# Optimization experiments

Measured on AMD Instinct MI355X. Metric: run time of the kernel, lower is better.

Reference implementation:

```python
import jax, jax.numpy as jnp
import numpy as np

N_NODES = 50000
N_EDGES = 800000
IN_DIM, HID_DIM, OUT_DIM = 128, 128, 64


def _sage_conv(x, src, dst, W_l, W_r, b, num_nodes):
    # mean aggregation of source-node features onto destination nodes
    msg = x[src]  # [E, d] gather
    summed = jax.ops.segment_sum(msg, dst, num_segments=num_nodes)  # [N, d]
    deg = jax.ops.segment_sum(jnp.ones((src.shape[0],), dtype=x.dtype), dst,
                              num_segments=num_nodes)  # [N]
    agg = summed / jnp.maximum(deg, 1.0)[:, None]
    # SAGEConv: lin_l(agg) + lin_r(x); bias only on lin_l (PyG default)
    return agg @ W_l + b + x @ W_r


def setup_inputs() -> dict:
    key = jax.random.key(0)
    k = jax.random.split(key, 8)
    def glorot(kk, shape):
        lim = float(np.sqrt(6.0 / (shape[0] + shape[1])))
        return jax.random.uniform(kk, shape, jnp.float32, -lim, lim)
    return {
        "x": jax.random.normal(k[0], (N_NODES, IN_DIM), jnp.float32),
        "edge_index": jax.random.randint(k[1], (2, N_EDGES), 0, N_NODES, jnp.int64),
        "W1_l": glorot(k[2], (IN_DIM, HID_DIM)),
        "W1_r": glorot(k[3], (IN_DIM, HID_DIM)),
        "b1": jnp.zeros((HID_DIM,), jnp.float32),
        "W2_l": glorot(k[4], (HID_DIM, OUT_DIM)),
        "W2_r": glorot(k[5], (HID_DIM, OUT_DIM)),
        "b2": jnp.zeros((OUT_DIM,), jnp.float32),
    }


def reference(x, edge_index, W1_l, W1_r, b1, W2_l, W2_r, b2):
    src, dst = edge_index[0], edge_index[1]
    n = x.shape[0]
    h = _sage_conv(x, src, dst, W1_l, W1_r, b1, n)
    h = jax.nn.relu(h)
    # dropout is identity in eval mode
    out = _sage_conv(h, src, dst, W2_l, W2_r, b2, n)
    return out
```

## Files before the change

kernel.cpp:

```cpp
#include <hip/hip_runtime.h>
#include <hip/hip_bf16.h>


#define BLK 256

typedef __attribute__((ext_vector_type(8))) short short8;
typedef __attribute__((ext_vector_type(4))) float f32x4;

__device__ inline unsigned short f2bf(float f) {
    unsigned int u = __builtin_bit_cast(unsigned int, f);
    u += 0x7fffu + ((u >> 16) & 1u);
    return (unsigned short)(u >> 16);
}
__device__ inline float bf2f(unsigned short h) {
    return __builtin_bit_cast(float, ((unsigned int)h) << 16);
}


__global__ __launch_bounds__(BLK) void deg_count_kernel(const int* __restrict__ dst,
                                                        int E, int* __restrict__ deg) {
    int e = blockIdx.x * BLK + threadIdx.x;
    if (e < E) atomicAdd(&deg[dst[e]], 1);
}

__global__ __launch_bounds__(BLK) void partial_sum_kernel(const int* __restrict__ deg,
                                                          int n, int* __restrict__ partials) {
    __shared__ int s[BLK];
    int t = threadIdx.x;
    int idx = blockIdx.x * BLK + t;
    s[t] = (idx < n) ? deg[idx] : 0;
    __syncthreads();
    for (int o = BLK / 2; o > 0; o >>= 1) {
        if (t < o) s[t] += s[t + o];
        __syncthreads();
    }
    if (t == 0) partials[blockIdx.x] = s[0];
}

__global__ __launch_bounds__(BLK) void scan_partials_kernel(int* __restrict__ partials, int n) {
    __shared__ int s[BLK];
    int t = threadIdx.x;
    int v = (t < n) ? partials[t] : 0;
    s[t] = v;
    __syncthreads();
    int sum = v;
    for (int o = 1; o < BLK; o <<= 1) {
        int other = (t >= o) ? s[t - o] : 0;
        __syncthreads();
        sum += other;
        s[t] = sum;
        __syncthreads();
    }
    if (t < n) partials[t] = sum - v;
}

__global__ __launch_bounds__(BLK) void chunk_scan_kernel(const int* __restrict__ deg,
                                                         const int* __restrict__ partials,
                                                         int n, int* __restrict__ row_start) {
    __shared__ int s[BLK];
    int t = threadIdx.x;
    int idx = blockIdx.x * BLK + t;
    int v = (idx < n) ? deg[idx] : 0;
    s[t] = v;
    __syncthreads();
    int sum = v;
    for (int o = 1; o < BLK; o <<= 1) {
        int other = (t >= o) ? s[t - o] : 0;
        __syncthreads();
        sum += other;
        s[t] = sum;
        __syncthreads();
    }
    if (idx < n) row_start[idx] = (sum - v) + partials[blockIdx.x];
}

__global__ __launch_bounds__(BLK) void fill_xcd_kernel(const int* __restrict__ src,
                                                       const int* __restrict__ dst, int E,
                                                       const int* __restrict__ row_start,
                                                       int* __restrict__ cursor,
                                                       int* __restrict__ csr_src,
                                                       int range, int CH) {
    const int oct = blockIdx.x & 7;
    const int chunk = blockIdx.x >> 3;
    const int lo = oct * range, hi = lo + range;
    int e0 = chunk * CH;
    int e1 = min(E, e0 + CH);
    for (int e = e0 + threadIdx.x; e < e1; e += BLK) {
        int d = dst[e];
        if (d >= lo && d < hi) {
            int pos = atomicAdd(&cursor[d], 1);
            csr_src[row_start[d] + pos] = src[e];
        }
    }
}


__global__ __launch_bounds__(BLK) void f32_to_bf16_kernel(const float* __restrict__ in,
                                                          unsigned short* __restrict__ out,
                                                          int nquad) {
    int i = blockIdx.x * BLK + threadIdx.x;
    if (i >= nquad) return;
    float4 v = ((const float4*)in)[i];
    ushort4 o;
    o.x = f2bf(v.x); o.y = f2bf(v.y); o.z = f2bf(v.z); o.w = f2bf(v.w);
    ((ushort4*)out)[i] = o;
}

__global__ __launch_bounds__(BLK) void pack_all_w_kernel(const float* __restrict__ W1l,
                                                         const float* __restrict__ W1r,
                                                         const float* __restrict__ W2l,
                                                         const float* __restrict__ W2r,
                                                         unsigned short* __restrict__ P1l,
                                                         unsigned short* __restrict__ P1r,
                                                         unsigned short* __restrict__ P2l,
                                                         unsigned short* __restrict__ P2r) {
    int t = blockIdx.x * BLK + threadIdx.x;
    const float* W;
    unsigned short* P;
    int Ncol, local;
    if (t < 16384)      { W = W1l; P = P1l; Ncol = 128; local = t; }
    else if (t < 32768) { W = W1r; P = P1r; Ncol = 128; local = t - 16384; }
    else if (t < 40960) { W = W2l; P = P2l; Ncol = 64;  local = t - 32768; }
    else if (t < 49152) { W = W2r; P = P2r; Ncol = 64;  local = t - 40960; }
    else return;
    int j = local & 7;
    int lane = (local >> 3) & 63;
    int rest = local >> 9;
    int nt = Ncol >> 4;
    int n16 = rest % nt, kb = rest / nt;
    int k = kb * 32 + (lane >> 4) * 8 + j;
    int c = n16 * 16 + (lane & 15);
    P[local] = f2bf(W[(size_t)k * Ncol + c]);
}


__global__ __launch_bounds__(BLK) void agg_mlp_kernel(const unsigned short* __restrict__ feat,
                                                      const int* __restrict__ row_start,
                                                      const int* __restrict__ deg,
                                                      const int* __restrict__ csr_src,
                                                      unsigned short* __restrict__ out,
                                                      int N, int E) {
    const int wave = threadIdx.x >> 6, lane = threadIdx.x & 63;
    const int node = blockIdx.x * (BLK / 64) + wave;
    if (node >= N) return;
    const int start = __builtin_amdgcn_readfirstlane(row_start[node]);
    int cnt = __builtin_amdgcn_readfirstlane(deg[node]);
    cnt = min(cnt, E);
    const float inv = 1.0f / fmaxf((float)cnt, 1.0f);
    const unsigned int* fp = (const unsigned int*)feat;

    float a0 = 0.f, a1 = 0.f;
    for (int base = 0; base < cnt; base += 64) {
        int m = cnt - base;
        if (m > 64) m = 64;
        int idxv = csr_src[start + base + (lane < m ? lane : m - 1)];
        for (int e = 0; e < m; e += 16) {
            unsigned int v[16];
#pragma unroll
            for (int j = 0; j < 16; j++) {
                int ee = e + j;
                int sl = ee < m ? ee : m - 1;
                int s = __builtin_amdgcn_readlane(idxv, sl);
                v[j] = fp[(size_t)s * 64 + lane];
            }
#pragma unroll
            for (int j = 0; j < 16; j++) {
                float w = (e + j < m) ? inv : 0.0f;
                a0 = fmaf(bf2f((unsigned short)v[j]), w, a0);
                a1 = fmaf(bf2f((unsigned short)(v[j] >> 16)), w, a1);
            }
        }
    }
    ((unsigned int*)out)[(size_t)node * 64 + lane] =
        (unsigned int)f2bf(a0) | ((unsigned int)f2bf(a1) << 16);
}


template <int NCOL, bool RELU, bool OUT_BF16>
__global__ __launch_bounds__(BLK) void gemm_dual_kernel(const unsigned short* __restrict__ A1,
                                                        const unsigned short* __restrict__ A2,
                                                        const unsigned short* __restrict__ Pl,
                                                        const unsigned short* __restrict__ Pr,
                                                        const float* __restrict__ bias,
                                                        void* __restrict__ outp, int M) {
    constexpr int NT = NCOL / 16;
    const int wave = threadIdx.x >> 6, lane = threadIdx.x & 63;
    const int r0 = blockIdx.x * 128 + wave * 32;
    const int arow = lane & 15, kgrp = lane >> 4;

    f32x4 acc[2][NT];
#pragma unroll
    for (int h = 0; h < 2; h++)
#pragma unroll
        for (int n = 0; n < NT; n++) acc[h][n] = (f32x4){0.f, 0.f, 0.f, 0.f};

    const int ra = min(r0 + arow, M - 1);
    const int rb = min(r0 + 16 + arow, M - 1);

#pragma unroll
    for (int mat = 0; mat < 2; ++mat) {
        const unsigned short* A = mat ? A2 : A1;
        const unsigned short* P = mat ? Pr : Pl;
        const unsigned short* Aa = A + (size_t)ra * 128 + kgrp * 8;
        const unsigned short* Ab = A + (size_t)rb * 128 + kgrp * 8;
#pragma unroll
        for (int kb = 0; kb < 4; ++kb) {
            short8 afa = *(const short8*)(Aa + kb * 32);
            short8 afb = *(const short8*)(Ab + kb * 32);
            const unsigned short* Pk = P + (size_t)kb * NT * 512 + lane * 8;
#pragma unroll
            for (int n = 0; n < NT; ++n) {
                short8 wf = *(const short8*)(Pk + n * 512);
                acc[0][n] = __builtin_amdgcn_mfma_f32_16x16x32_bf16(afa, wf, acc[0][n], 0, 0, 0);
                acc[1][n] = __builtin_amdgcn_mfma_f32_16x16x32_bf16(afb, wf, acc[1][n], 0, 0, 0);
            }
        }
    }

#pragma unroll
    for (int n = 0; n < NT; ++n) {
        int col = n * 16 + arow;
        float bv = bias[col];
#pragma unroll
        for (int h = 0; h < 2; ++h) {
#pragma unroll
            for (int i = 0; i < 4; ++i) {
                int row = r0 + h * 16 + kgrp * 4 + i;
                if (row < M) {
                    float v = acc[h][n][i] + bv;
                    if (RELU) v = fmaxf(v, 0.f);
                    if (OUT_BF16)
                        ((unsigned short*)outp)[(size_t)row * NCOL + col] = f2bf(v);
                    else
                        ((float*)outp)[(size_t)row * NCOL + col] = v;
                }
            }
        }
    }
}


extern "C" void kernel_launch(void* const* d_in, const int* in_sizes, int n_in,
                              void* d_out, int out_size, void* d_ws, size_t ws_size,
                              hipStream_t stream) {
    const float* x   = (const float*)d_in[0];
    const int*   ei  = (const int*)d_in[1];
    const float* W1l = (const float*)d_in[2];
    const float* W1r = (const float*)d_in[3];
    const float* b1  = (const float*)d_in[4];
    const float* W2l = (const float*)d_in[5];
    const float* W2r = (const float*)d_in[6];
    const float* b2  = (const float*)d_in[7];
    float* out = (float*)d_out;

    const int N = in_sizes[0] / 128;
    const int E = in_sizes[1] / 2;
    const int* src = ei;
    const int* dst = ei + E;

    char* ws = (char*)d_ws;
    size_t off = 0;
    auto carve = [&](size_t bytes) {
        void* p = ws + off;
        off += (bytes + 255) & ~(size_t)255;
        return p;
    };
    int* deg       = (int*)carve((size_t)2 * N * 4);
    int* cursor    = deg + N;
    int* row_start = (int*)carve((size_t)N * 4);
    int* partials  = (int*)carve(256 * 4);
    int* csr_src   = (int*)carve((size_t)E * 4);
    unsigned short* xb   = (unsigned short*)carve((size_t)N * 128 * 2);
    unsigned short* aggb = (unsigned short*)carve((size_t)N * 128 * 2);
    unsigned short* hb   = (unsigned short*)carve((size_t)N * 128 * 2);
    unsigned short* P1l  = (unsigned short*)carve(128 * 128 * 2);
    unsigned short* P1r  = (unsigned short*)carve(128 * 128 * 2);
    unsigned short* P2l  = (unsigned short*)carve(128 * 64 * 2);
    unsigned short* P2r  = (unsigned short*)carve(128 * 64 * 2);

    hipMemsetAsync(deg, 0, (size_t)2 * N * 4, stream);

    const int nquad = N * 128 / 4;
    f32_to_bf16_kernel<<<(nquad + BLK - 1) / BLK, BLK, 0, stream>>>(x, xb, nquad);
    pack_all_w_kernel<<<192, BLK, 0, stream>>>(W1l, W1r, W2l, W2r, P1l, P1r, P2l, P2r);

    const int nchunk = (N + BLK - 1) / BLK;
    deg_count_kernel<<<(E + BLK - 1) / BLK, BLK, 0, stream>>>(dst, E, deg);
    partial_sum_kernel<<<nchunk, BLK, 0, stream>>>(deg, N, partials);
    scan_partials_kernel<<<1, BLK, 0, stream>>>(partials, nchunk);
    chunk_scan_kernel<<<nchunk, BLK, 0, stream>>>(deg, partials, N, row_start);

    const int range = (N + 7) / 8;
    const int NCHUNKS = 512;
    const int CH = (E + NCHUNKS - 1) / NCHUNKS;
    fill_xcd_kernel<<<8 * NCHUNKS, BLK, 0, stream>>>(src, dst, E, row_start, cursor,
                                                     csr_src, range, CH);

    const int aggGrid = (N + 3) / 4;
    const int gemmGrid = (N + 127) / 128;

    agg_mlp_kernel<<<aggGrid, BLK, 0, stream>>>(xb, row_start, deg, csr_src, aggb, N, E);
    gemm_dual_kernel<128, true, true><<<gemmGrid, BLK, 0, stream>>>(aggb, xb, P1l, P1r, b1, hb, N);
    agg_mlp_kernel<<<aggGrid, BLK, 0, stream>>>(hb, row_start, deg, csr_src, aggb, N, E);
    gemm_dual_kernel<64, false, false><<<gemmGrid, BLK, 0, stream>>>(aggb, hb, P2l, P2r, b2, out, N);
}
```

Before: 265.5 us.

## Slice node features into per-XCD planes for L2-local gather aggregation

Stores bf16 node features as four 32-column planes ([slice][node][32]) and maps aggregation blocks so each XCD (blockIdx & 7) handles one slice and one half of the nodes. The intent is to keep each XCD's random gather working set small enough to stay in its local L2 instead of thrashing across the whole 12.8MB feature table. Each wave now processes four edges per load step using 16-lane groups, then reduces across groups with shuffles. The degree count is also XCD-partitioned like the CSR fill, and x conversion is fused with weight packing into one prep kernel. GEMM kernels are adapted to read and write the planar layout, which costs strided writes and a cross-lane reduction.

```diff
diff --git a/kernel.cpp b/kernel.cpp
--- a/kernel.cpp
+++ b/kernel.cpp
@@ -17,10 +17,18 @@
 }
 
 
-__global__ __launch_bounds__(BLK) void deg_count_kernel(const int* __restrict__ dst,
-                                                        int E, int* __restrict__ deg) {
-    int e = blockIdx.x * BLK + threadIdx.x;
-    if (e < E) atomicAdd(&deg[dst[e]], 1);
+__global__ __launch_bounds__(BLK) void deg_xcd_kernel(const int* __restrict__ dst, int E,
+                                                      int* __restrict__ deg,
+                                                      int range, int CH) {
+    const int oct = blockIdx.x & 7;
+    const int chunk = blockIdx.x >> 3;
+    const int lo = oct * range, hi = lo + range;
+    int e0 = chunk * CH;
+    int e1 = min(E, e0 + CH);
+    for (int e = e0 + threadIdx.x; e < e1; e += BLK) {
+        int d = dst[e];
+        if (d >= lo && d < hi) atomicAdd(&deg[d], 1);
+    }
 }
 
 __global__ __launch_bounds__(BLK) void partial_sum_kernel(const int* __restrict__ deg,
@@ -95,33 +103,42 @@
 }
 
 
-__global__ __launch_bounds__(BLK) void f32_to_bf16_kernel(const float* __restrict__ in,
-                                                          unsigned short* __restrict__ out,
-                                                          int nquad) {
-    int i = blockIdx.x * BLK + threadIdx.x;
-    if (i >= nquad) return;
-    float4 v = ((const float4*)in)[i];
-    ushort4 o;
-    o.x = f2bf(v.x); o.y = f2bf(v.y); o.z = f2bf(v.z); o.w = f2bf(v.w);
-    ((ushort4*)out)[i] = o;
-}
-
-__global__ __launch_bounds__(BLK) void pack_all_w_kernel(const float* __restrict__ W1l,
-                                                         const float* __restrict__ W1r,
-                                                         const float* __restrict__ W2l,
-                                                         const float* __restrict__ W2r,
-                                                         unsigned short* __restrict__ P1l,
-                                                         unsigned short* __restrict__ P1r,
-                                                         unsigned short* __restrict__ P2l,
-                                                         unsigned short* __restrict__ P2r) {
+__global__ __launch_bounds__(BLK) void prep_kernel(const float* __restrict__ x,
+                                                   unsigned short* __restrict__ xT, int N,
+                                                   const float* __restrict__ W1l,
+                                                   const float* __restrict__ W1r,
+                                                   const float* __restrict__ W2l,
+                                                   const float* __restrict__ W2r,
+                                                   unsigned short* __restrict__ P1l,
+                                                   unsigned short* __restrict__ P1r,
+                                                   unsigned short* __restrict__ P2l,
+                                                   unsigned short* __restrict__ P2r) {
     int t = blockIdx.x * BLK + threadIdx.x;
+    const int NX = N * 4;
+    if (t < NX) {
+        int node = t >> 2, slice = t & 3;
+        const float4* xp = (const float4*)(x + (size_t)node * 128 + slice * 32);
+        unsigned int u[16];
+#pragma unroll
+        for (int q = 0; q < 8; ++q) {
+            float4 v = xp[q];
+            u[q * 2]     = (unsigned int)f2bf(v.x) | ((unsigned int)f2bf(v.y) << 16);
+            u[q * 2 + 1] = (unsigned int)f2bf(v.z) | ((unsigned int)f2bf(v.w) << 16);
+        }
+        uint4* o = (uint4*)(xT + ((size_t)slice * N + node) * 32);
+#pragma unroll
+        for (int q = 0; q < 4; ++q)
+            o[q] = make_uint4(u[q * 4], u[q * 4 + 1], u[q * 4 + 2], u[q * 4 + 3]);
+        return;
+    }
+    int w = t - NX;
     const float* W;
     unsigned short* P;
     int Ncol, local;
-    if (t < 16384)      { W = W1l; P = P1l; Ncol = 128; local = t; }
-    else if (t < 32768) { W = W1r; P = P1r; Ncol = 128; local = t - 16384; }
-    else if (t < 40960) { W = W2l; P = P2l; Ncol = 64;  local = t - 32768; }
-    else if (t < 49152) { W = W2r; P = P2r; Ncol = 64;  local = t - 40960; }
+    if (w < 16384)      { W = W1l; P = P1l; Ncol = 128; local = w; }
+    else if (w < 32768) { W = W1r; P = P1r; Ncol = 128; local = w - 16384; }
+    else if (w < 40960) { W = W2l; P = P2l; Ncol = 64;  local = w - 32768; }
+    else if (w < 49152) { W = W2r; P = P2r; Ncol = 64;  local = w - 40960; }
     else return;
     int j = local & 7;
     int lane = (local >> 3) & 63;
@@ -134,55 +151,68 @@
 }
 
 
-__global__ __launch_bounds__(BLK) void agg_mlp_kernel(const unsigned short* __restrict__ feat,
-                                                      const int* __restrict__ row_start,
-                                                      const int* __restrict__ deg,
-                                                      const int* __restrict__ csr_src,
-                                                      unsigned short* __restrict__ out,
-                                                      int N, int E) {
+__global__ __launch_bounds__(BLK) void agg4_kernel(const unsigned short* __restrict__ fT,
+                                                   const int* __restrict__ row_start,
+                                                   const int* __restrict__ deg,
+                                                   const int* __restrict__ csr_src,
+                                                   unsigned short* __restrict__ aT,
+                                                   int N, int E) {
     const int wave = threadIdx.x >> 6, lane = threadIdx.x & 63;
-    const int node = blockIdx.x * (BLK / 64) + wave;
-    if (node >= N) return;
+    const int oct = blockIdx.x & 7;
+    const int k = blockIdx.x >> 3;
+    const int slice = oct >> 1, half = oct & 1;
+    const int halfSize = (N + 1) >> 1;
+    const int node = half * halfSize + k * 4 + wave;
+    if (node >= N || node >= (half + 1) * halfSize) return;
+
     const int start = __builtin_amdgcn_readfirstlane(row_start[node]);
     int cnt = __builtin_amdgcn_readfirstlane(deg[node]);
     cnt = min(cnt, E);
     const float inv = 1.0f / fmaxf((float)cnt, 1.0f);
-    const unsigned int* fp = (const unsigned int*)feat;
+
+    const unsigned int* xs = (const unsigned int*)(fT + (size_t)slice * N * 32);
+    const int cu = lane & 15;
+    const int sub = lane >> 4;
 
     float a0 = 0.f, a1 = 0.f;
     for (int base = 0; base < cnt; base += 64) {
         int m = cnt - base;
         if (m > 64) m = 64;
         int idxv = csr_src[start + base + (lane < m ? lane : m - 1)];
-        for (int e = 0; e < m; e += 16) {
-            unsigned int v[16];
-#pragma unroll
-            for (int j = 0; j < 16; j++) {
-                int ee = e + j;
-                int sl = ee < m ? ee : m - 1;
-                int s = __builtin_amdgcn_readlane(idxv, sl);
-                v[j] = fp[(size_t)s * 64 + lane];
+        for (int e = 0; e < m; e += 32) {
+            unsigned int v[8];
+            float wgt[8];
+#pragma unroll
+            for (int j = 0; j < 8; j++) {
+                int slot = e + j * 4 + sub;
+                wgt[j] = (slot < m) ? inv : 0.0f;
+                int sl = slot < m ? slot : m - 1;
+                int s = __shfl(idxv, sl);
+                v[j] = xs[(size_t)s * 16 + cu];
             }
 #pragma unroll
-            for (int j = 0; j < 16; j++) {
-                float w = (e + j < m) ? inv : 0.0f;
-                a0 = fmaf(bf2f((unsigned short)v[j]), w, a0);
-                a1 = fmaf(bf2f((unsigned short)(v[j] >> 16)), w, a1);
+            for (int j = 0; j < 8; j++) {
+                a0 = fmaf(bf2f((unsigned short)v[j]), wgt[j], a0);
+                a1 = fmaf(bf2f((unsigned short)(v[j] >> 16)), wgt[j], a1);
             }
         }
     }
-    ((unsigned int*)out)[(size_t)node * 64 + lane] =
-        (unsigned int)f2bf(a0) | ((unsigned int)f2bf(a1) << 16);
-}
-
-
-template <int NCOL, bool RELU, bool OUT_BF16>
-__global__ __launch_bounds__(BLK) void gemm_dual_kernel(const unsigned short* __restrict__ A1,
-                                                        const unsigned short* __restrict__ A2,
-                                                        const unsigned short* __restrict__ Pl,
-                                                        const unsigned short* __restrict__ Pr,
-                                                        const float* __restrict__ bias,
-                                                        void* __restrict__ outp, int M) {
+    a0 += __shfl_xor(a0, 16); a1 += __shfl_xor(a1, 16);
+    a0 += __shfl_xor(a0, 32); a1 += __shfl_xor(a1, 32);
+    if (sub == 0) {
+        unsigned int* as = (unsigned int*)(aT + (size_t)slice * N * 32);
+        as[(size_t)node * 16 + cu] = (unsigned int)f2bf(a0) | ((unsigned int)f2bf(a1) << 16);
+    }
+}
+
+
+template <int NCOL, bool RELU, int OUTMODE>
+__global__ __launch_bounds__(BLK) void gemm_dual_T_kernel(const unsigned short* __restrict__ A1,
+                                                          const unsigned short* __restrict__ A2,
+                                                          const unsigned short* __restrict__ Pl,
+                                                          const unsigned short* __restrict__ Pr,
+                                                          const float* __restrict__ bias,
+                                                          void* __restrict__ outp, int M) {
     constexpr int NT = NCOL / 16;
     const int wave = threadIdx.x >> 6, lane = threadIdx.x & 63;
     const int r0 = blockIdx.x * 128 + wave * 32;
@@ -196,17 +226,18 @@
 
     const int ra = min(r0 + arow, M - 1);
     const int rb = min(r0 + 16 + arow, M - 1);
+    const size_t plane = (size_t)M * 32;
 
 #pragma unroll
     for (int mat = 0; mat < 2; ++mat) {
         const unsigned short* A = mat ? A2 : A1;
         const unsigned short* P = mat ? Pr : Pl;
-        const unsigned short* Aa = A + (size_t)ra * 128 + kgrp * 8;
-        const unsigned short* Ab = A + (size_t)rb * 128 + kgrp * 8;
+        const unsigned short* Aa = A + (size_t)ra * 32 + kgrp * 8;
+        const unsigned short* Ab = A + (size_t)rb * 32 + kgrp * 8;
 #pragma unroll
         for (int kb = 0; kb < 4; ++kb) {
-            short8 afa = *(const short8*)(Aa + kb * 32);
-            short8 afb = *(const short8*)(Ab + kb * 32);
+            short8 afa = *(const short8*)(Aa + (size_t)kb * plane);
+            short8 afb = *(const short8*)(Ab + (size_t)kb * plane);
             const unsigned short* Pk = P + (size_t)kb * NT * 512 + lane * 8;
 #pragma unroll
             for (int n = 0; n < NT; ++n) {
@@ -229,10 +260,13 @@
                 if (row < M) {
                     float v = acc[h][n][i] + bv;
                     if (RELU) v = fmaxf(v, 0.f);
-                    if (OUT_BF16)
-                        ((unsigned short*)outp)[(size_t)row * NCOL + col] = f2bf(v);
-                    else
+                    if (OUTMODE == 1) {
+                        int sl = col >> 5, c32 = col & 31;
+                        ((unsigned short*)outp)[(size_t)sl * M * 32 + (size_t)row * 32 + c32] =
+                            f2bf(v);
+                    } else {
                         ((float*)outp)[(size_t)row * NCOL + col] = v;
+                    }
                 }
             }
         }
@@ -270,9 +304,9 @@
     int* row_start = (int*)carve((size_t)N * 4);
     int* partials  = (int*)carve(256 * 4);
     int* csr_src   = (int*)carve((size_t)E * 4);
-    unsigned short* xb   = (unsigned short*)carve((size_t)N * 128 * 2);
-    unsigned short* aggb = (unsigned short*)carve((size_t)N * 128 * 2);
-    unsigned short* hb   = (unsigned short*)carve((size_t)N * 128 * 2);
+    unsigned short* xT   = (unsigned short*)carve((size_t)4 * N * 32 * 2);
+    unsigned short* hT   = (unsigned short*)carve((size_t)4 * N * 32 * 2);
+    unsigned short* aggT = (unsigned short*)carve((size_t)4 * N * 32 * 2);
     unsigned short* P1l  = (unsigned short*)carve(128 * 128 * 2);
     unsigned short* P1r  = (unsigned short*)carve(128 * 128 * 2);
     unsigned short* P2l  = (unsigned short*)carve(128 * 64 * 2);
@@ -280,27 +314,29 @@
 
     hipMemsetAsync(deg, 0, (size_t)2 * N * 4, stream);
 
-    const int nquad = N * 128 / 4;
-    f32_to_bf16_kernel<<<(nquad + BLK - 1) / BLK, BLK, 0, stream>>>(x, xb, nquad);
-    pack_all_w_kernel<<<192, BLK, 0, stream>>>(W1l, W1r, W2l, W2r, P1l, P1r, P2l, P2r);
+    const int prepThreads = N * 4 + 49152;
+    prep_kernel<<<(prepThreads + BLK - 1) / BLK, BLK, 0, stream>>>(
+        x, xT, N, W1l, W1r, W2l, W2r, P1l, P1r, P2l, P2r);
+
+    const int range = (N + 7) / 8;
+    const int NCHUNKS = 512;
+    const int CH = (E + NCHUNKS - 1) / NCHUNKS;
+    deg_xcd_kernel<<<8 * NCHUNKS, BLK, 0, stream>>>(dst, E, deg, range, CH);
 
     const int nchunk = (N + BLK - 1) / BLK;
-    deg_count_kernel<<<(E + BLK - 1) / BLK, BLK, 0, stream>>>(dst, E, deg);
     partial_sum_kernel<<<nchunk, BLK, 0, stream>>>(deg, N, partials);
     scan_partials_kernel<<<1, BLK, 0, stream>>>(partials, nchunk);
     chunk_scan_kernel<<<nchunk, BLK, 0, stream>>>(deg, partials, N, row_start);
 
-    const int range = (N + 7) / 8;
-    const int NCHUNKS = 512;
-    const int CH = (E + NCHUNKS - 1) / NCHUNKS;
     fill_xcd_kernel<<<8 * NCHUNKS, BLK, 0, stream>>>(src, dst, E, row_start, cursor,
                                                      csr_src, range, CH);
 
-    const int aggGrid = (N + 3) / 4;
+    const int halfSize = (N + 1) >> 1;
+    const int aggGrid = 8 * ((halfSize + 3) / 4);
     const int gemmGrid = (N + 127) / 128;
 
-    agg_mlp_kernel<<<aggGrid, BLK, 0, stream>>>(xb, row_start, deg, csr_src, aggb, N, E);
-    gemm_dual_kernel<128, true, true><<<gemmGrid, BLK, 0, stream>>>(aggb, xb, P1l, P1r, b1, hb, N);
-    agg_mlp_kernel<<<aggGrid, BLK, 0, stream>>>(hb, row_start, deg, csr_src, aggb, N, E);
-    gemm_dual_kernel<64, false, false><<<gemmGrid, BLK, 0, stream>>>(aggb, hb, P2l, P2r, b2, out, N);
-}
+    agg4_kernel<<<aggGrid, BLK, 0, stream>>>(xT, row_start, deg, csr_src, aggT, N, E);
+    gemm_dual_T_kernel<128, true, 1><<<gemmGrid, BLK, 0, stream>>>(aggT, xT, P1l, P1r, b1, hT, N);
+    agg4_kernel<<<aggGrid, BLK, 0, stream>>>(hT, row_start, deg, csr_src, aggT, N, E);
+    gemm_dual_T_kernel<64, false, 0><<<gemmGrid, BLK, 0, stream>>>(aggT, hT, P2l, P2r, b2, out, N);
+}
```

Result: slower. 317.7 us (+19.7%).

## Switch aggregation to edge-parallel segmented reduction with fp32 atomics

Applied to the files above, without the earlier changes.

Replaces the per-node gather aggregation with an edge-parallel kernel where each wave handles 64 CSR-sorted edges, reduces runs of equal destination in registers, and flushes scaled partial sums via float atomics into an fp32 buffer. The GEMM now reads the fp32 aggregate and converts to bf16 on load. Degree counting is split by destination range per XCD, inverse degrees are precomputed in the scan, and the input and weight conversion kernels are fused. This trades per-node load imbalance for extra memsets, a csr_dst array, doubled aggregate bytes, and atomic contention.

```diff
diff --git a/kernel.cpp b/kernel.cpp
--- a/kernel.cpp
+++ b/kernel.cpp
@@ -5,6 +5,7 @@
 #define BLK 256
 
 typedef __attribute__((ext_vector_type(8))) short short8;
+typedef __attribute__((ext_vector_type(8))) unsigned short ushort8;
 typedef __attribute__((ext_vector_type(4))) float f32x4;
 
 __device__ inline unsigned short f2bf(float f) {
@@ -17,10 +18,18 @@
 }
 
 
-__global__ __launch_bounds__(BLK) void deg_count_kernel(const int* __restrict__ dst,
-                                                        int E, int* __restrict__ deg) {
-    int e = blockIdx.x * BLK + threadIdx.x;
-    if (e < E) atomicAdd(&deg[dst[e]], 1);
+__global__ __launch_bounds__(BLK) void deg_xcd_kernel(const int* __restrict__ dst, int E,
+                                                      int* __restrict__ deg,
+                                                      int range, int CH) {
+    const int oct = blockIdx.x & 7;
+    const int chunk = blockIdx.x >> 3;
+    const int lo = oct * range, hi = lo + range;
+    int e0 = chunk * CH;
+    int e1 = min(E, e0 + CH);
+    for (int e = e0 + threadIdx.x; e < e1; e += BLK) {
+        int d = dst[e];
+        if (d >= lo && d < hi) atomicAdd(&deg[d], 1);
+    }
 }
 
 __global__ __launch_bounds__(BLK) void partial_sum_kernel(const int* __restrict__ deg,
@@ -56,7 +65,8 @@
 
 __global__ __launch_bounds__(BLK) void chunk_scan_kernel(const int* __restrict__ deg,
                                                          const int* __restrict__ partials,
-                                                         int n, int* __restrict__ row_start) {
+                                                         int n, int* __restrict__ row_start,
+                                                         float* __restrict__ inv_deg) {
     __shared__ int s[BLK];
     int t = threadIdx.x;
     int idx = blockIdx.x * BLK + t;
@@ -71,7 +81,10 @@
         s[t] = sum;
         __syncthreads();
     }
-    if (idx < n) row_start[idx] = (sum - v) + partials[blockIdx.x];
+    if (idx < n) {
+        row_start[idx] = (sum - v) + partials[blockIdx.x];
+        inv_deg[idx] = 1.0f / fmaxf((float)v, 1.0f);
+    }
 }
 
 __global__ __launch_bounds__(BLK) void fill_xcd_kernel(const int* __restrict__ src,
@@ -79,6 +92,7 @@
                                                        const int* __restrict__ row_start,
                                                        int* __restrict__ cursor,
                                                        int* __restrict__ csr_src,
+                                                       int* __restrict__ csr_dst,
                                                        int range, int CH) {
     const int oct = blockIdx.x & 7;
     const int chunk = blockIdx.x >> 3;
@@ -89,39 +103,40 @@
         int d = dst[e];
         if (d >= lo && d < hi) {
             int pos = atomicAdd(&cursor[d], 1);
-            csr_src[row_start[d] + pos] = src[e];
-        }
-    }
-}
-
-
-__global__ __launch_bounds__(BLK) void f32_to_bf16_kernel(const float* __restrict__ in,
-                                                          unsigned short* __restrict__ out,
-                                                          int nquad) {
-    int i = blockIdx.x * BLK + threadIdx.x;
-    if (i >= nquad) return;
-    float4 v = ((const float4*)in)[i];
-    ushort4 o;
-    o.x = f2bf(v.x); o.y = f2bf(v.y); o.z = f2bf(v.z); o.w = f2bf(v.w);
-    ((ushort4*)out)[i] = o;
-}
-
-__global__ __launch_bounds__(BLK) void pack_all_w_kernel(const float* __restrict__ W1l,
-                                                         const float* __restrict__ W1r,
-                                                         const float* __restrict__ W2l,
-                                                         const float* __restrict__ W2r,
-                                                         unsigned short* __restrict__ P1l,
-                                                         unsigned short* __restrict__ P1r,
-                                                         unsigned short* __restrict__ P2l,
-                                                         unsigned short* __restrict__ P2r) {
+            int p = row_start[d] + pos;
+            csr_src[p] = src[e];
+            csr_dst[p] = d;
+        }
+    }
+}
+
+
+__global__ __launch_bounds__(BLK) void prep_kernel(const float* __restrict__ x,
+                                                   unsigned short* __restrict__ xb, int nquad,
+                                                   const float* __restrict__ W1l,
+                                                   const float* __restrict__ W1r,
+                                                   const float* __restrict__ W2l,
+                                                   const float* __restrict__ W2r,
+                                                   unsigned short* __restrict__ P1l,
+                                                   unsigned short* __restrict__ P1r,
+                                                   unsigned short* __restrict__ P2l,
+                                                   unsigned short* __restrict__ P2r) {
     int t = blockIdx.x * BLK + threadIdx.x;
+    if (t < nquad) {
+        float4 v = ((const float4*)x)[t];
+        ushort4 o;
+        o.x = f2bf(v.x); o.y = f2bf(v.y); o.z = f2bf(v.z); o.w = f2bf(v.w);
+        ((ushort4*)xb)[t] = o;
+        return;
+    }
+    int w = t - nquad;
     const float* W;
     unsigned short* P;
     int Ncol, local;
-    if (t < 16384)      { W = W1l; P = P1l; Ncol = 128; local = t; }
-    else if (t < 32768) { W = W1r; P = P1r; Ncol = 128; local = t - 16384; }
-    else if (t < 40960) { W = W2l; P = P2l; Ncol = 64;  local = t - 32768; }
-    else if (t < 49152) { W = W2r; P = P2r; Ncol = 64;  local = t - 40960; }
+    if (w < 16384)      { W = W1l; P = P1l; Ncol = 128; local = w; }
+    else if (w < 32768) { W = W1r; P = P1r; Ncol = 128; local = w - 16384; }
+    else if (w < 40960) { W = W2l; P = P2l; Ncol = 64;  local = w - 32768; }
+    else if (w < 49152) { W = W2r; P = P2r; Ncol = 64;  local = w - 40960; }
     else return;
     int j = local & 7;
     int lane = (local >> 3) & 63;
@@ -134,50 +149,67 @@
 }
 
 
-__global__ __launch_bounds__(BLK) void agg_mlp_kernel(const unsigned short* __restrict__ feat,
-                                                      const int* __restrict__ row_start,
-                                                      const int* __restrict__ deg,
-                                                      const int* __restrict__ csr_src,
-                                                      unsigned short* __restrict__ out,
-                                                      int N, int E) {
+__global__ __launch_bounds__(BLK) void agg_edge_kernel(const unsigned short* __restrict__ feat,
+                                                       const int* __restrict__ csr_src,
+                                                       const int* __restrict__ csr_dst,
+                                                       const float* __restrict__ inv_deg,
+                                                       float* __restrict__ aggf, int E) {
     const int wave = threadIdx.x >> 6, lane = threadIdx.x & 63;
-    const int node = blockIdx.x * (BLK / 64) + wave;
-    if (node >= N) return;
-    const int start = __builtin_amdgcn_readfirstlane(row_start[node]);
-    int cnt = __builtin_amdgcn_readfirstlane(deg[node]);
-    cnt = min(cnt, E);
-    const float inv = 1.0f / fmaxf((float)cnt, 1.0f);
+    const int e0 = (blockIdx.x * (BLK / 64) + wave) * 64;
+    if (e0 >= E) return;
+    int m = E - e0 < 64 ? E - e0 : 64;
+    int srcv = csr_src[e0 + (lane < m ? lane : m - 1)];
+    int dstv = csr_dst[e0 + (lane < m ? lane : m - 1)];
     const unsigned int* fp = (const unsigned int*)feat;
 
+    int d_cur = __builtin_amdgcn_readlane(dstv, 0);
     float a0 = 0.f, a1 = 0.f;
-    for (int base = 0; base < cnt; base += 64) {
-        int m = cnt - base;
-        if (m > 64) m = 64;
-        int idxv = csr_src[start + base + (lane < m ? lane : m - 1)];
-        for (int e = 0; e < m; e += 16) {
-            unsigned int v[16];
-#pragma unroll
-            for (int j = 0; j < 16; j++) {
-                int ee = e + j;
-                int sl = ee < m ? ee : m - 1;
-                int s = __builtin_amdgcn_readlane(idxv, sl);
-                v[j] = fp[(size_t)s * 64 + lane];
+
+#pragma unroll
+    for (int b = 0; b < 64; b += 16) {
+        int bm = m - b;
+        if (bm <= 0) break;
+        if (bm > 16) bm = 16;
+        unsigned int v[16];
+#pragma unroll
+        for (int j = 0; j < 16; j++) {
+            int sl = b + (j < bm ? j : bm - 1);
+            int s = __builtin_amdgcn_readlane(srcv, sl);
+            v[j] = fp[(size_t)s * 64 + lane];
+        }
+#pragma unroll
+        for (int j = 0; j < 16; j++) {
+            if (j < bm) {
+                int d = __builtin_amdgcn_readlane(dstv, b + j);
+                if (d != d_cur) {
+                    float inv = inv_deg[d_cur];
+                    atomicAdd(&aggf[(size_t)d_cur * 128 + lane * 2],     a0 * inv);
+                    atomicAdd(&aggf[(size_t)d_cur * 128 + lane * 2 + 1], a1 * inv);
+                    d_cur = d;
+                    a0 = 0.f; a1 = 0.f;
+                }
+                a0 += bf2f((unsigned short)v[j]);
+                a1 += bf2f((unsigned short)(v[j] >> 16));
             }
-#pragma unroll
-            for (int j = 0; j < 16; j++) {
-                float w = (e + j < m) ? inv : 0.0f;
-                a0 = fmaf(bf2f((unsigned short)v[j]), w, a0);
-                a1 = fmaf(bf2f((unsigned short)(v[j] >> 16)), w, a1);
-            }
-        }
-    }
-    ((unsigned int*)out)[(size_t)node * 64 + lane] =
-        (unsigned int)f2bf(a0) | ((unsigned int)f2bf(a1) << 16);
-}
-
+        }
+    }
+    float inv = inv_deg[d_cur];
+    atomicAdd(&aggf[(size_t)d_cur * 128 + lane * 2],     a0 * inv);
+    atomicAdd(&aggf[(size_t)d_cur * 128 + lane * 2 + 1], a1 * inv);
+}
+
+
+__device__ inline short8 ld_a_f32(const float* __restrict__ A, int row, int kbase) {
+    const float4* p = (const float4*)(A + (size_t)row * 128 + kbase);
+    float4 x0 = p[0], x1 = p[1];
+    ushort8 r;
+    r[0] = f2bf(x0.x); r[1] = f2bf(x0.y); r[2] = f2bf(x0.z); r[3] = f2bf(x0.w);
+    r[4] = f2bf(x1.x); r[5] = f2bf(x1.y); r[6] = f2bf(x1.z); r[7] = f2bf(x1.w);
+    return __builtin_bit_cast(short8, r);
+}
 
 template <int NCOL, bool RELU, bool OUT_BF16>
-__global__ __launch_bounds__(BLK) void gemm_dual_kernel(const unsigned short* __restrict__ A1,
+__global__ __launch_bounds__(BLK) void gemm_dual_kernel(const float* __restrict__ A1f,
                                                         const unsigned short* __restrict__ A2,
                                                         const unsigned short* __restrict__ Pl,
                                                         const unsigned short* __restrict__ Pr,
@@ -198,16 +230,25 @@
     const int rb = min(r0 + 16 + arow, M - 1);
 
 #pragma unroll
-    for (int mat = 0; mat < 2; ++mat) {
-        const unsigned short* A = mat ? A2 : A1;
-        const unsigned short* P = mat ? Pr : Pl;
-        const unsigned short* Aa = A + (size_t)ra * 128 + kgrp * 8;
-        const unsigned short* Ab = A + (size_t)rb * 128 + kgrp * 8;
+    for (int kb = 0; kb < 4; ++kb) {
+        short8 afa = ld_a_f32(A1f, ra, kgrp * 8 + kb * 32);
+        short8 afb = ld_a_f32(A1f, rb, kgrp * 8 + kb * 32);
+        const unsigned short* Pk = Pl + (size_t)kb * NT * 512 + lane * 8;
+#pragma unroll
+        for (int n = 0; n < NT; ++n) {
+            short8 wf = *(const short8*)(Pk + n * 512);
+            acc[0][n] = __builtin_amdgcn_mfma_f32_16x16x32_bf16(afa, wf, acc[0][n], 0, 0, 0);
+            acc[1][n] = __builtin_amdgcn_mfma_f32_16x16x32_bf16(afb, wf, acc[1][n], 0, 0, 0);
+        }
+    }
+    {
+        const unsigned short* Aa = A2 + (size_t)ra * 128 + kgrp * 8;
+        const unsigned short* Ab = A2 + (size_t)rb * 128 + kgrp * 8;
 #pragma unroll
         for (int kb = 0; kb < 4; ++kb) {
             short8 afa = *(const short8*)(Aa + kb * 32);
             short8 afb = *(const short8*)(Ab + kb * 32);
-            const unsigned short* Pk = P + (size_t)kb * NT * 512 + lane * 8;
+            const unsigned short* Pk = Pr + (size_t)kb * NT * 512 + lane * 8;
 #pragma unroll
             for (int n = 0; n < NT; ++n) {
                 short8 wf = *(const short8*)(Pk + n * 512);
@@ -268,39 +309,44 @@
     int* deg       = (int*)carve((size_t)2 * N * 4);
     int* cursor    = deg + N;
     int* row_start = (int*)carve((size_t)N * 4);
+    float* inv_deg = (float*)carve((size_t)N * 4);
     int* partials  = (int*)carve(256 * 4);
     int* csr_src   = (int*)carve((size_t)E * 4);
-    unsigned short* xb   = (unsigned short*)carve((size_t)N * 128 * 2);
-    unsigned short* aggb = (unsigned short*)carve((size_t)N * 128 * 2);
-    unsigned short* hb   = (unsigned short*)carve((size_t)N * 128 * 2);
-    unsigned short* P1l  = (unsigned short*)carve(128 * 128 * 2);
-    unsigned short* P1r  = (unsigned short*)carve(128 * 128 * 2);
-    unsigned short* P2l  = (unsigned short*)carve(128 * 64 * 2);
-    unsigned short* P2r  = (unsigned short*)carve(128 * 64 * 2);
+    int* csr_dst   = (int*)carve((size_t)E * 4);
+    unsigned short* xb = (unsigned short*)carve((size_t)N * 128 * 2);
+    unsigned short* hb = (unsigned short*)carve((size_t)N * 128 * 2);
+    float* aggf        = (float*)carve((size_t)N * 128 * 4);
+    unsigned short* P1l = (unsigned short*)carve(128 * 128 * 2);
+    unsigned short* P1r = (unsigned short*)carve(128 * 128 * 2);
+    unsigned short* P2l = (unsigned short*)carve(128 * 64 * 2);
+    unsigned short* P2r = (unsigned short*)carve(128 * 64 * 2);
 
     hipMemsetAsync(deg, 0, (size_t)2 * N * 4, stream);
+    hipMemsetAsync(aggf, 0, (size_t)N * 128 * 4, stream);
 
     const int nquad = N * 128 / 4;
-    f32_to_bf16_kernel<<<(nquad + BLK - 1) / BLK, BLK, 0, stream>>>(x, xb, nquad);
-    pack_all_w_kernel<<<192, BLK, 0, stream>>>(W1l, W1r, W2l, W2r, P1l, P1r, P2l, P2r);
-
-    const int nchunk = (N + BLK - 1) / BLK;
-    deg_count_kernel<<<(E + BLK - 1) / BLK, BLK, 0, stream>>>(dst, E, deg);
-    partial_sum_kernel<<<nchunk, BLK, 0, stream>>>(deg, N, partials);
-    scan_partials_kernel<<<1, BLK, 0, stream>>>(partials, nchunk);
-    chunk_scan_kernel<<<nchunk, BLK, 0, stream>>>(deg, partials, N, row_start);
+    prep_kernel<<<(nquad + 49152 + BLK - 1) / BLK, BLK, 0, stream>>>(
+        x, xb, nquad, W1l, W1r, W2l, W2r, P1l, P1r, P2l, P2r);
 
     const int range = (N + 7) / 8;
     const int NCHUNKS = 512;
     const int CH = (E + NCHUNKS - 1) / NCHUNKS;
+    deg_xcd_kernel<<<8 * NCHUNKS, BLK, 0, stream>>>(dst, E, deg, range, CH);
+
+    const int nchunk = (N + BLK - 1) / BLK;
+    partial_sum_kernel<<<nchunk, BLK, 0, stream>>>(deg, N, partials);
+    scan_partials_kernel<<<1, BLK, 0, stream>>>(partials, nchunk);
+    chunk_scan_kernel<<<nchunk, BLK, 0, stream>>>(deg, partials, N, row_start, inv_deg);
+
     fill_xcd_kernel<<<8 * NCHUNKS, BLK, 0, stream>>>(src, dst, E, row_start, cursor,
-                                                     csr_src, range, CH);
-
-    const int aggGrid = (N + 3) / 4;
+                                                     csr_src, csr_dst, range, CH);
+
+    const int aggGrid = (E / 64 + 3) / 4;
     const int gemmGrid = (N + 127) / 128;
 
-    agg_mlp_kernel<<<aggGrid, BLK, 0, stream>>>(xb, row_start, deg, csr_src, aggb, N, E);
-    gemm_dual_kernel<128, true, true><<<gemmGrid, BLK, 0, stream>>>(aggb, xb, P1l, P1r, b1, hb, N);
-    agg_mlp_kernel<<<aggGrid, BLK, 0, stream>>>(hb, row_start, deg, csr_src, aggb, N, E);
-    gemm_dual_kernel<64, false, false><<<gemmGrid, BLK, 0, stream>>>(aggb, hb, P2l, P2r, b2, out, N);
-}
+    agg_edge_kernel<<<aggGrid, BLK, 0, stream>>>(xb, csr_src, csr_dst, inv_deg, aggf, E);
+    gemm_dual_kernel<128, true, true><<<gemmGrid, BLK, 0, stream>>>(aggf, xb, P1l, P1r, b1, hb, N);
+    hipMemsetAsync(aggf, 0, (size_t)N * 128 * 4, stream);
+    agg_edge_kernel<<<aggGrid, BLK, 0, stream>>>(hb, csr_src, csr_dst, inv_deg, aggf, E);
+    gemm_dual_kernel<64, false, false><<<gemmGrid, BLK, 0, stream>>>(aggf, hb, P2l, P2r, b2, out, N);
+}
```

Measured after the change: 344.8 us. 1.3x slower.

## Fuse three-kernel scan into single-pass scan and merge prep kernels

Applied to the files above, without the earlier changes.

Replaces the partial-sum, partial-scan and chunk-scan kernels with one scan kernel. Each block publishes its total with a release flag, then spins on the flags of all earlier blocks and reduces their sums to get its base offset. The bf16 conversion of x and the weight packing are also merged into one launch. The aim is to cut kernel launches and inter-kernel gaps, at the cost of spin-waiting that relies on earlier blocks making forward progress (196 blocks fit on the device).

```diff
diff --git a/kernel.cpp b/kernel.cpp
--- a/kernel.cpp
+++ b/kernel.cpp
@@ -23,43 +23,13 @@
     if (e < E) atomicAdd(&deg[dst[e]], 1);
 }
 
-__global__ __launch_bounds__(BLK) void partial_sum_kernel(const int* __restrict__ deg,
-                                                          int n, int* __restrict__ partials) {
+__global__ __launch_bounds__(BLK) void scan_fused_kernel(const int* __restrict__ deg, int n,
+                                                         int* __restrict__ row_start,
+                                                         int* __restrict__ bsum,
+                                                         int* __restrict__ bflag) {
     __shared__ int s[BLK];
-    int t = threadIdx.x;
-    int idx = blockIdx.x * BLK + t;
-    s[t] = (idx < n) ? deg[idx] : 0;
-    __syncthreads();
-    for (int o = BLK / 2; o > 0; o >>= 1) {
-        if (t < o) s[t] += s[t + o];
-        __syncthreads();
-    }
-    if (t == 0) partials[blockIdx.x] = s[0];
-}
-
-__global__ __launch_bounds__(BLK) void scan_partials_kernel(int* __restrict__ partials, int n) {
-    __shared__ int s[BLK];
-    int t = threadIdx.x;
-    int v = (t < n) ? partials[t] : 0;
-    s[t] = v;
-    __syncthreads();
-    int sum = v;
-    for (int o = 1; o < BLK; o <<= 1) {
-        int other = (t >= o) ? s[t - o] : 0;
-        __syncthreads();
-        sum += other;
-        s[t] = sum;
-        __syncthreads();
-    }
-    if (t < n) partials[t] = sum - v;
-}
-
-__global__ __launch_bounds__(BLK) void chunk_scan_kernel(const int* __restrict__ deg,
-                                                         const int* __restrict__ partials,
-                                                         int n, int* __restrict__ row_start) {
-    __shared__ int s[BLK];
-    int t = threadIdx.x;
-    int idx = blockIdx.x * BLK + t;
+    const int t = threadIdx.x, b = blockIdx.x;
+    const int idx = b * BLK + t;
     int v = (idx < n) ? deg[idx] : 0;
     s[t] = v;
     __syncthreads();
@@ -71,7 +41,25 @@
         s[t] = sum;
         __syncthreads();
     }
-    if (idx < n) row_start[idx] = (sum - v) + partials[blockIdx.x];
+    int total = s[BLK - 1];
+    if (t == 0) {
+        __hip_atomic_store(&bsum[b], total, __ATOMIC_RELAXED, __HIP_MEMORY_SCOPE_AGENT);
+        __hip_atomic_store(&bflag[b], 1, __ATOMIC_RELEASE, __HIP_MEMORY_SCOPE_AGENT);
+    }
+    __syncthreads();
+    int pred = 0;
+    if (t < b) {
+        while (__hip_atomic_load(&bflag[t], __ATOMIC_ACQUIRE, __HIP_MEMORY_SCOPE_AGENT) == 0) {}
+        pred = __hip_atomic_load(&bsum[t], __ATOMIC_RELAXED, __HIP_MEMORY_SCOPE_AGENT);
+    }
+    s[t] = pred;
+    __syncthreads();
+    for (int o = BLK / 2; o > 0; o >>= 1) {
+        if (t < o) s[t] += s[t + o];
+        __syncthreads();
+    }
+    const int base = s[0];
+    if (idx < n) row_start[idx] = base + sum - v;
 }
 
 __global__ __launch_bounds__(BLK) void fill_xcd_kernel(const int* __restrict__ src,
@@ -95,33 +83,32 @@
 }
 
 
-__global__ __launch_bounds__(BLK) void f32_to_bf16_kernel(const float* __restrict__ in,
-                                                          unsigned short* __restrict__ out,
-                                                          int nquad) {
-    int i = blockIdx.x * BLK + threadIdx.x;
-    if (i >= nquad) return;
-    float4 v = ((const float4*)in)[i];
-    ushort4 o;
-    o.x = f2bf(v.x); o.y = f2bf(v.y); o.z = f2bf(v.z); o.w = f2bf(v.w);
-    ((ushort4*)out)[i] = o;
-}
-
-__global__ __launch_bounds__(BLK) void pack_all_w_kernel(const float* __restrict__ W1l,
-                                                         const float* __restrict__ W1r,
-                                                         const float* __restrict__ W2l,
-                                                         const float* __restrict__ W2r,
-                                                         unsigned short* __restrict__ P1l,
-                                                         unsigned short* __restrict__ P1r,
-                                                         unsigned short* __restrict__ P2l,
-                                                         unsigned short* __restrict__ P2r) {
+__global__ __launch_bounds__(BLK) void prep_kernel(const float* __restrict__ x,
+                                                   unsigned short* __restrict__ xb, int nquad,
+                                                   const float* __restrict__ W1l,
+                                                   const float* __restrict__ W1r,
+                                                   const float* __restrict__ W2l,
+                                                   const float* __restrict__ W2r,
+                                                   unsigned short* __restrict__ P1l,
+                                                   unsigned short* __restrict__ P1r,
+                                                   unsigned short* __restrict__ P2l,
+                                                   unsigned short* __restrict__ P2r) {
     int t = blockIdx.x * BLK + threadIdx.x;
+    if (t < nquad) {
+        float4 v = ((const float4*)x)[t];
+        ushort4 o;
+        o.x = f2bf(v.x); o.y = f2bf(v.y); o.z = f2bf(v.z); o.w = f2bf(v.w);
+        ((ushort4*)xb)[t] = o;
+        return;
+    }
+    int w = t - nquad;
     const float* W;
     unsigned short* P;
     int Ncol, local;
-    if (t < 16384)      { W = W1l; P = P1l; Ncol = 128; local = t; }
-    else if (t < 32768) { W = W1r; P = P1r; Ncol = 128; local = t - 16384; }
-    else if (t < 40960) { W = W2l; P = P2l; Ncol = 64;  local = t - 32768; }
-    else if (t < 49152) { W = W2r; P = P2r; Ncol = 64;  local = t - 40960; }
+    if (w < 16384)      { W = W1l; P = P1l; Ncol = 128; local = w; }
+    else if (w < 32768) { W = W1r; P = P1r; Ncol = 128; local = w - 16384; }
+    else if (w < 40960) { W = W2l; P = P2l; Ncol = 64;  local = w - 32768; }
+    else if (w < 49152) { W = W2r; P = P2r; Ncol = 64;  local = w - 40960; }
     else return;
     int j = local & 7;
     int lane = (local >> 3) & 63;
@@ -265,10 +252,11 @@
         off += (bytes + 255) & ~(size_t)255;
         return p;
     };
-    int* deg       = (int*)carve((size_t)2 * N * 4);
+    int* deg       = (int*)carve((size_t)(2 * N + 512) * 4);
     int* cursor    = deg + N;
+    int* bflag     = deg + 2 * N;
+    int* bsum      = bflag + 256;
     int* row_start = (int*)carve((size_t)N * 4);
-    int* partials  = (int*)carve(256 * 4);
     int* csr_src   = (int*)carve((size_t)E * 4);
     unsigned short* xb   = (unsigned short*)carve((size_t)N * 128 * 2);
     unsigned short* aggb = (unsigned short*)carve((size_t)N * 128 * 2);
@@ -278,17 +266,16 @@
     unsigned short* P2l  = (unsigned short*)carve(128 * 64 * 2);
     unsigned short* P2r  = (unsigned short*)carve(128 * 64 * 2);
 
-    hipMemsetAsync(deg, 0, (size_t)2 * N * 4, stream);
+    hipMemsetAsync(deg, 0, (size_t)(2 * N + 256) * 4, stream);
 
     const int nquad = N * 128 / 4;
-    f32_to_bf16_kernel<<<(nquad + BLK - 1) / BLK, BLK, 0, stream>>>(x, xb, nquad);
-    pack_all_w_kernel<<<192, BLK, 0, stream>>>(W1l, W1r, W2l, W2r, P1l, P1r, P2l, P2r);
+    prep_kernel<<<(nquad + 49152 + BLK - 1) / BLK, BLK, 0, stream>>>(
+        x, xb, nquad, W1l, W1r, W2l, W2r, P1l, P1r, P2l, P2r);
+
+    deg_count_kernel<<<(E + BLK - 1) / BLK, BLK, 0, stream>>>(dst, E, deg);
 
     const int nchunk = (N + BLK - 1) / BLK;
-    deg_count_kernel<<<(E + BLK - 1) / BLK, BLK, 0, stream>>>(dst, E, deg);
-    partial_sum_kernel<<<nchunk, BLK, 0, stream>>>(deg, N, partials);
-    scan_partials_kernel<<<1, BLK, 0, stream>>>(partials, nchunk);
-    chunk_scan_kernel<<<nchunk, BLK, 0, stream>>>(deg, partials, N, row_start);
+    scan_fused_kernel<<<nchunk, BLK, 0, stream>>>(deg, N, row_start, bsum, bflag);
 
     const int range = (N + 7) / 8;
     const int NCHUNKS = 512;
```

After: 272.0 us. 1.02x slower.
